# Optimization experiments

Hardware: AMD Instinct MI355X
Metric: run time of the kernel (lower is better)

The kernel has to match this reference:

```python
import jax, jax.numpy as jnp
import numpy as np

POOL = 7  # RoIPooling output size (7,7)


def roi_pool(x, img, rois):
    """RoIPool matching the torch loop: scale rois to feature coords, truncate to int,
    take inclusive slice [y1:y2+1, x1:x2+1] and AdaptiveMaxPool2d((7,7)).
    x: [1,C,H,W], img: [1,3,h,w], rois: [N,4] (x1,y1,x2,y2 in image coords).
    Returns [N,C,7,7]."""
    _, C, H, W = x.shape
    h_img, w_img = img.shape[2], img.shape[3]
    scale = jnp.array([W / w_img, H / h_img, W / w_img, H / h_img], jnp.float32)
    r = (rois * scale).astype(jnp.int32)  # .long() truncation (coords >= 0)
    x1 = jnp.clip(r[:, 0], 0, W - 1)
    y1 = jnp.clip(r[:, 1], 0, H - 1)
    x2 = jnp.clip(r[:, 2], 0, W - 1)
    y2 = jnp.clip(r[:, 3], 0, H - 1)
    ww = x2 - x1 + 1  # inclusive slice width
    hh = y2 - y1 + 1
    i = jnp.arange(POOL)
    # AdaptiveMaxPool bin boundaries: start=floor(i*L/7), end=ceil((i+1)*L/7)  -> [N,7]
    col_s = x1[:, None] + (i[None, :] * ww[:, None]) // POOL
    col_e = x1[:, None] + ((i[None, :] + 1) * ww[:, None] + POOL - 1) // POOL
    row_s = y1[:, None] + (i[None, :] * hh[:, None]) // POOL
    row_e = y1[:, None] + ((i[None, :] + 1) * hh[:, None] + POOL - 1) // POOL
    wpos = jnp.arange(W)
    hpos = jnp.arange(H)
    colmask = (wpos[None, None, :] >= col_s[:, :, None]) & (wpos[None, None, :] < col_e[:, :, None])  # [N,7,W]
    rowmask = (hpos[None, None, :] >= row_s[:, :, None]) & (hpos[None, None, :] < row_e[:, :, None])  # [N,7,H]
    feat = x[0]  # [C,H,W]
    neg = jnp.asarray(jnp.finfo(feat.dtype).min, feat.dtype)
    def per_roi(masks):
        rm, cm = masks  # [7,H], [7,W]
        # separable max over the rectangular bin: cols first, then rows
        t = jnp.max(jnp.where(cm[None, None, :, :], feat[:, :, None, :], neg), axis=-1)  # [C,H,7]
        return jnp.max(jnp.where(rm[None, :, :, None], t[:, None, :, :], neg), axis=2)  # [C,7,7]
    return jax.lax.map(per_roi, (rowmask, colmask))  # [N,C,7,7]


def setup_inputs() -> dict:
    key = jax.random.key(0)
    ks = jax.random.split(key, 10)
    C, H, W = 512, 50, 50
    h_img, w_img = 800, 800
    N = 512
    num_classes = 20
    x = jax.random.normal(ks[0], (1, C, H, W), jnp.float32)
    img = jnp.zeros((1, 3, h_img, w_img), jnp.float32)
    bx = jax.random.uniform(ks[1], (N,), minval=0.0, maxval=w_img - 320.0)
    by = jax.random.uniform(ks[2], (N,), minval=0.0, maxval=h_img - 320.0)
    bw = jax.random.uniform(ks[3], (N,), minval=32.0, maxval=320.0)
    bh = jax.random.uniform(ks[4], (N,), minval=32.0, maxval=320.0)
    rois = jnp.stack([bx, by, bx + bw, by + bh], axis=1).astype(jnp.float32)
    D = C * POOL * POOL  # 25088
    W1 = jax.random.normal(ks[5], (D, 4096), jnp.float32) / np.sqrt(D)
    b1 = jnp.zeros((4096,), jnp.float32)
    W2 = jax.random.normal(ks[6], (4096, 4096), jnp.float32) / np.sqrt(4096)
    b2 = jnp.zeros((4096,), jnp.float32)
    Wcls = jax.random.normal(ks[7], (4096, num_classes + 1), jnp.float32) / np.sqrt(4096)
    bcls = jnp.zeros((num_classes + 1,), jnp.float32)
    Wreg = jax.random.normal(ks[8], (4096, 4 * (num_classes + 1)), jnp.float32) / np.sqrt(4096)
    breg = jnp.zeros((4 * (num_classes + 1),), jnp.float32)
    return {"x": x, "img": img, "rois": rois, "W1": W1, "b1": b1, "W2": W2,
            "b2": b2, "Wcls": Wcls, "bcls": bcls, "Wreg": Wreg, "breg": breg}


def reference(x, img, rois, W1, b1, W2, b2, Wcls, bcls, Wreg, breg):
    pooled = roi_pool(x, img, rois)                 # [N,C,7,7]
    f = pooled.reshape(pooled.shape[0], -1)          # flatten -> [N,25088]
    f = jax.nn.relu(f @ W1 + b1)                     # fc_head layer 1
    f = jax.nn.relu(f @ W2 + b2)                     # fc_head layer 2
    y_cls = f @ Wcls + bcls                          # [N, num_classes+1]
    y_reg = f @ Wreg + breg                          # [N, 4*(num_classes+1)]
    return (y_cls, y_reg)
```

## Files before the change

kernel.cpp:

```cpp
#include <hip/hip_runtime.h>


typedef __attribute__((ext_vector_type(8))) __bf16 bf16x8;
typedef __attribute__((ext_vector_type(4))) float f32x4;

#define N_ROIS 512
#define FH 50
#define FW 50
#define KK1 25088
#define D1 4096
#define BK 32

__device__ __forceinline__ void gll16(const void* g, void* l) {
  __builtin_amdgcn_global_load_lds(
      (const __attribute__((address_space(1))) void*)g,
      (__attribute__((address_space(3))) void*)l, 16, 0, 0);
}

__global__ __launch_bounds__(256) void roipool_kernel(
    const float* __restrict__ x, const float* __restrict__ rois,
    __bf16* __restrict__ pooled) {
  const int bid = blockIdx.x;
  const int roi = bid >> 3;
  const int cg = bid & 7;
  const float s = 0.0625f;
  const float r0 = rois[roi * 4 + 0], r1 = rois[roi * 4 + 1];
  const float r2 = rois[roi * 4 + 2], r3 = rois[roi * 4 + 3];
  int x1 = (int)(r0 * s); x1 = min(max(x1, 0), FW - 1);
  int y1 = (int)(r1 * s); y1 = min(max(y1, 0), FH - 1);
  int x2 = (int)(r2 * s); x2 = min(max(x2, 0), FW - 1);
  int y2 = (int)(r3 * s); y2 = min(max(y2, 0), FH - 1);
  const int ww = x2 - x1 + 1, hh = y2 - y1 + 1;
  __shared__ int cs[7], ce[7], rs[7], re[7];
  if (threadIdx.x < 7) {
    int i = threadIdx.x;
    cs[i] = x1 + (i * ww) / 7;
    ce[i] = x1 + ((i + 1) * ww + 6) / 7;
    rs[i] = y1 + (i * hh) / 7;
    re[i] = y1 + ((i + 1) * hh + 6) / 7;
  }
  __syncthreads();
  for (int idx = threadIdx.x; idx < 64 * 49; idx += 256) {
    int cl = idx / 49;
    int p = idx - cl * 49;
    int py = p / 7, px = p - py * 7;
    const int c = cg * 64 + cl;
    const float* base = x + (size_t)c * (FH * FW);
    float m = -3.402823466e38f;
    for (int y = rs[py]; y < re[py]; ++y) {
      const float* rowp = base + y * FW;
      for (int xx = cs[px]; xx < ce[px]; ++xx) m = fmaxf(m, rowp[xx]);
    }
    pooled[(size_t)roi * KK1 + c * 49 + p] = (__bf16)m;
  }
}

template <typename OutT>
__global__ __launch_bounds__(256, 1) void gemm_pipe(
    const __bf16* __restrict__ A, const float* __restrict__ B,
    OutT* __restrict__ part, int N, int K, int kslice, int npad, int zshift) {
  __shared__ float Blds[4][32 * 128];
  const int tid = threadIdx.x;
  const int lane = tid & 63;
  const int w = tid >> 6;
  const int bid = blockIdx.x;
  const int z = bid & ((1 << zshift) - 1);
  const int n0 = (bid >> zshift) * 128;
  const int kbeg = z * kslice;
  const int niters = kslice / BK;
  const int fr = lane & 15;
  const int ks = lane >> 4;

  f32x4 acc[8][8];
#pragma unroll
  for (int i = 0; i < 8; ++i)
#pragma unroll
    for (int j = 0; j < 8; ++j) acc[i][j] = (f32x4){0.f, 0.f, 0.f, 0.f};

  const __bf16* Abase = A + (size_t)(w * 128 + fr) * K + kbeg + ks * 8;
  const size_t Astride = (size_t)16 * K;

  const int srow = w * 8 + (lane >> 5);
  const float* Bsrc = B + n0 + (((lane & 31) ^ (2 * w)) << 2);

  bf16x8 af[8];

#define STAGE(t)                                                          \
  {                                                                       \
    int off = (t) * BK;                                                   \
    if (off >= kslice) off = 0;    \
    _Pragma("unroll") for (int i = 0; i < 4; ++i) {                       \
      gll16((const void*)(Bsrc + (size_t)(kbeg + off + srow + 2 * i) * N),\
            (void*)&Blds[(t) & 3][(w * 8 + 2 * i) * 128]);                \
    }                                                                     \
  }

#define RD8(P, nf_)                                                       \
  {                                                                       \
    const int base_ = (ks * 8) * 128 +                                    \
        ((((nf_) * 4 + (fr >> 2)) ^ (2 * ks)) << 2) + (fr & 3);           \
    P##0 = bl[base_];        P##1 = bl[base_ + 128];                      \
    P##2 = bl[base_ + 256];  P##3 = bl[base_ + 384];                      \
    P##4 = bl[base_ + 512];  P##5 = bl[base_ + 640];                      \
    P##6 = bl[base_ + 768];  P##7 = bl[base_ + 896];                      \
  }

#define MM8(P, nf_)                                                       \
  {                                                                       \
    bf16x8 bfr;                                                           \
    bfr[0] = (__bf16)P##0; bfr[1] = (__bf16)P##1;                         \
    bfr[2] = (__bf16)P##2; bfr[3] = (__bf16)P##3;                         \
    bfr[4] = (__bf16)P##4; bfr[5] = (__bf16)P##5;                         \
    bfr[6] = (__bf16)P##6; bfr[7] = (__bf16)P##7;                         \
    _Pragma("unroll") for (int mf = 0; mf < 8; ++mf)                      \
        acc[mf][nf_] = __builtin_amdgcn_mfma_f32_16x16x32_bf16(           \
            af[mf], bfr, acc[mf][nf_], 0, 0, 0);                          \
  }

  STAGE(0);
  STAGE(1);

  for (int it = 0; it < niters; ++it) {
    {
      const __bf16* ap = Abase + (size_t)it * BK;
#pragma unroll
      for (int i = 0; i < 8; ++i)
        af[i] = *(const bf16x8*)(ap + (size_t)i * Astride);
    }
    STAGE(it + 2);
    asm volatile("s_waitcnt vmcnt(16)" ::: "memory");
    __builtin_amdgcn_s_barrier();
    __builtin_amdgcn_sched_barrier(0);

    const float* bl = &Blds[it & 3][0];
    float rA0, rA1, rA2, rA3, rA4, rA5, rA6, rA7;
    float rB0, rB1, rB2, rB3, rB4, rB5, rB6, rB7;
    float rC0, rC1, rC2, rC3, rC4, rC5, rC6, rC7;
    RD8(rA, 0);
    RD8(rB, 1);
    RD8(rC, 2); MM8(rA, 0);
    RD8(rA, 3); MM8(rB, 1);
    RD8(rB, 4); MM8(rC, 2);
    RD8(rC, 5); MM8(rA, 3);
    RD8(rA, 6); MM8(rB, 4);
    RD8(rB, 7); MM8(rC, 5);
    MM8(rA, 6);
    MM8(rB, 7);
  }
#undef MM8
#undef RD8
#undef STAGE

  const int r0 = ks * 4;
  OutT* pbase = part + (size_t)z * 512 * npad;
#pragma unroll
  for (int mf = 0; mf < 8; ++mf)
#pragma unroll
    for (int nf = 0; nf < 8; ++nf) {
      const int col = n0 + nf * 16 + fr;
#pragma unroll
      for (int r = 0; r < 4; ++r) {
        const int row = w * 128 + mf * 16 + r0 + r;
        pbase[(size_t)row * npad + col] = (OutT)acc[mf][nf][r];
      }
    }
}

template <typename OutT>
__global__ __launch_bounds__(256, 1) void gemm_small(
    const __bf16* __restrict__ A, const float* __restrict__ B,
    OutT* __restrict__ part, int N, int K, int kslice, int npad, int zshift) {
  const int tid = threadIdx.x;
  const int lane = tid & 63;
  const int w = tid >> 6;
  const int bid = blockIdx.x;
  const int z = bid & ((1 << zshift) - 1);
  const int n0 = (bid >> zshift) * 64;
  const int kbeg = z * kslice;
  const int niters = kslice / BK;
  const int kmax = kbeg + kslice;
  const int fr = lane & 15;
  const int ks = lane >> 4;
  const int m0 = w * 128;
  const bool fullN = (n0 + 64) <= N;

  f32x4 acc[8][4];
#pragma unroll
  for (int i = 0; i < 8; ++i)
#pragma unroll
    for (int j = 0; j < 4; ++j) acc[i][j] = (f32x4){0.f, 0.f, 0.f, 0.f};

  const __bf16* Abase = A + (size_t)(m0 + fr) * K + ks * 8;
  const size_t Astride = (size_t)16 * K;
  const float* Bbase = B + n0 + fr;

  bf16x8 afA[8], afB[8];
  float bA[32], bB[32];

#define LOAD_A(D, t)                                                     \
  {                                                                      \
    int kk = kbeg + (t) * BK;                                            \
    if (kk >= kmax) kk = kbeg;                                           \
    const __bf16* ap = Abase + kk;                                       \
    _Pragma("unroll") for (int i = 0; i < 8; ++i)                        \
        D[i] = *(const bf16x8*)(ap + (size_t)i * Astride);               \
  }

#define LOAD_B(S, t)                                                     \
  {                                                                      \
    int kg = kbeg + (t) * BK;                                            \
    if (kg >= kmax) kg = kbeg;                                           \
    const float* p = Bbase + (size_t)(kg + ks * 8) * N;                  \
    if (fullN) {                                                         \
      _Pragma("unroll") for (int e = 0; e < 8; ++e) {                    \
        _Pragma("unroll") for (int nf = 0; nf < 4; ++nf)                 \
            S[e * 4 + nf] = p[nf * 16];                                  \
        p += N;                                                          \
      }                                                                  \
    } else {                                                             \
      _Pragma("unroll") for (int e = 0; e < 8; ++e) {                    \
        _Pragma("unroll") for (int nf = 0; nf < 4; ++nf)                 \
            S[e * 4 + nf] =                                              \
                (n0 + nf * 16 + fr < N) ? p[nf * 16] : 0.f;              \
        p += N;                                                          \
      }                                                                  \
    }                                                                    \
  }

#define BODY(it, CA, NA, CB)                                             \
  {                                                                      \
    bf16x8 bfr[4];                                                       \
    _Pragma("unroll") for (int e = 0; e < 8; ++e)                        \
        _Pragma("unroll") for (int nf = 0; nf < 4; ++nf)                 \
            bfr[nf][e] = (__bf16)CB[e * 4 + nf];                         \
    LOAD_B(CB, (it) + 2);                                                \
    LOAD_A(NA, (it) + 1);                                                \
    _Pragma("unroll") for (int nf = 0; nf < 4; ++nf)                     \
        _Pragma("unroll") for (int mf = 0; mf < 8; ++mf)                 \
            acc[mf][nf] = __builtin_amdgcn_mfma_f32_16x16x32_bf16(       \
                CA[mf], bfr[nf], acc[mf][nf], 0, 0, 0);                  \
  }

  LOAD_A(afA, 0);
  LOAD_B(bA, 0);
  LOAD_B(bB, 1);
  for (int it = 0; it < niters; it += 2) {
    BODY(it, afA, afB, bA);
    BODY(it + 1, afB, afA, bB);
  }
#undef BODY
#undef LOAD_B
#undef LOAD_A

  const int r0 = ks * 4;
  OutT* pbase = part + (size_t)z * 512 * npad;
#pragma unroll
  for (int mf = 0; mf < 8; ++mf)
#pragma unroll
    for (int nf = 0; nf < 4; ++nf) {
      const int col = n0 + nf * 16 + fr;
#pragma unroll
      for (int r = 0; r < 4; ++r) {
        const int row = m0 + mf * 16 + r0 + r;
        pbase[(size_t)row * npad + col] = (OutT)acc[mf][nf][r];
      }
    }
}

__global__ __launch_bounds__(256) void reduce_relu_kernel(
    const __bf16* __restrict__ part, const float* __restrict__ bias,
    __bf16* __restrict__ out, int nsplit) {
  const int idx = blockIdx.x * 256 + threadIdx.x;
  const int flat = idx * 8;
  if (flat >= 512 * 4096) return;
  float s[8];
#pragma unroll
  for (int j = 0; j < 8; ++j) s[j] = 0.f;
  for (int sp = 0; sp < nsplit; ++sp) {
    bf16x8 v = *(const bf16x8*)(part + (size_t)sp * (512 * 4096) + flat);
#pragma unroll
    for (int j = 0; j < 8; ++j) s[j] += (float)v[j];
  }
  const int nb = flat & 4095;
  bf16x8 o;
#pragma unroll
  for (int j = 0; j < 8; ++j) {
    float v = s[j] + bias[nb + j];
    o[j] = (__bf16)(v > 0.f ? v : 0.f);
  }
  *(bf16x8*)(out + flat) = o;
}

__global__ __launch_bounds__(256) void reduce_out_kernel(
    const float* __restrict__ pc, const float* __restrict__ pr,
    const float* __restrict__ bcls, const float* __restrict__ breg,
    float* __restrict__ out, int nsplit) {
  const int gid = blockIdx.x * 256 + threadIdx.x;
  if (gid >= 512 * 105) return;
  if (gid < 512 * 21) {
    const int m = gid / 21, j = gid - m * 21;
    float s = bcls[j];
    for (int sp = 0; sp < nsplit; ++sp)
      s += pc[(size_t)sp * 512 * 128 + m * 128 + j];
    out[gid] = s;
  } else {
    const int g = gid - 512 * 21;
    const int m = g / 84, j = g - m * 84;
    float s = breg[j];
    for (int sp = 0; sp < nsplit; ++sp)
      s += pr[(size_t)sp * 512 * 128 + m * 128 + j];
    out[gid] = s;
  }
}

extern "C" void kernel_launch(void* const* d_in, const int* in_sizes, int n_in,
                              void* d_out, int out_size, void* d_ws, size_t ws_size,
                              hipStream_t stream) {
  (void)in_sizes; (void)n_in; (void)out_size;
  const float* x    = (const float*)d_in[0];
  const float* rois = (const float*)d_in[2];
  const float* W1   = (const float*)d_in[3];
  const float* b1   = (const float*)d_in[4];
  const float* W2   = (const float*)d_in[5];
  const float* b2   = (const float*)d_in[6];
  const float* Wcls = (const float*)d_in[7];
  const float* bcls = (const float*)d_in[8];
  const float* Wreg = (const float*)d_in[9];
  const float* breg = (const float*)d_in[10];
  float* out = (float*)d_out;

  const size_t pooled_b = (size_t)512 * KK1 * 2;
  const size_t act_b = (size_t)512 * D1 * 2;
  const size_t need8 = pooled_b + (size_t)8 * act_b + 2 * act_b;
  const int ns = (ws_size >= need8) ? 8 : 2;
  const int zshift = (ns == 8) ? 3 : 1;

  char* ws = (char*)d_ws;
  __bf16* pooled = (__bf16*)ws;
  __bf16* part1 = (__bf16*)(ws + pooled_b);
  __bf16* f1 = (__bf16*)(ws + pooled_b + (size_t)ns * act_b);
  __bf16* f2 = (__bf16*)(ws + pooled_b + (size_t)ns * act_b + act_b);
  __bf16* part2 = (__bf16*)ws;
  float* pcls = (float*)ws;
  float* preg = (float*)(ws + (size_t)64 * 512 * 128 * 4);

  roipool_kernel<<<N_ROIS * 8, 256, 0, stream>>>(x, rois, pooled);

  gemm_pipe<__bf16><<<32 * ns, 256, 0, stream>>>(
      pooled, W1, part1, 4096, KK1, KK1 / ns, 4096, zshift);
  reduce_relu_kernel<<<1024, 256, 0, stream>>>(part1, b1, f1, ns);

  gemm_pipe<__bf16><<<32 * ns, 256, 0, stream>>>(
      f1, W2, part2, 4096, 4096, 4096 / ns, 4096, zshift);
  reduce_relu_kernel<<<1024, 256, 0, stream>>>(part2, b2, f2, ns);

  gemm_small<float><<<64, 256, 0, stream>>>(
      f2, Wcls, pcls, 21, 4096, 64, 128, 6);
  gemm_small<float><<<128, 256, 0, stream>>>(
      f2, Wreg, preg, 84, 4096, 64, 128, 6);
  reduce_out_kernel<<<(512 * 105 + 255) / 256, 256, 0, stream>>>(
      pcls, preg, bcls, breg, out, 64);
}
```

Baseline: 340.6 us.

## Stage A tiles through double-buffered LDS with async global-to-LDS loads

The A operand (bf16 pooled features) is now brought into a swizzled, double-buffered LDS tile using `global_load_lds`, one stage ahead. Previously it was loaded straight from global memory into registers at the top of every iteration. This is meant to hide A-load latency behind the MFMA work and free registers. The existing `vmcnt` wait now also covers the A stage. The cost is 64KB more LDS per block and extra ds_read traffic for the A fragments.

```diff
diff --git a/kernel.cpp b/kernel.cpp
--- a/kernel.cpp
+++ b/kernel.cpp
@@ -60,6 +60,7 @@
     const __bf16* __restrict__ A, const float* __restrict__ B,
     OutT* __restrict__ part, int N, int K, int kslice, int npad, int zshift) {
   __shared__ float Blds[4][32 * 128];
+  __shared__ __bf16 A_lds[2][512 * 32];
   const int tid = threadIdx.x;
   const int lane = tid & 63;
   const int w = tid >> 6;
@@ -77,15 +78,27 @@
 #pragma unroll
     for (int j = 0; j < 8; ++j) acc[i][j] = (f32x4){0.f, 0.f, 0.f, 0.f};
 
-  const __bf16* Abase = A + (size_t)(w * 128 + fr) * K + kbeg + ks * 8;
-  const size_t Astride = (size_t)16 * K;
+  const int aswz = (lane & 3) ^ ((lane >> 2) & 3) ^ ((lane >> 4) & 3);
+  const __bf16* Asrc =
+      A + (size_t)(w * 128 + (lane >> 2)) * K + kbeg + aswz * 8;
+  const int aslot = ks ^ ((fr & 3) ^ ((fr >> 2) & 3));
 
   const int srow = w * 8 + (lane >> 5);
   const float* Bsrc = B + n0 + (((lane & 31) ^ (2 * w)) << 2);
 
   bf16x8 af[8];
 
-#define STAGE(t)                                                          \
+#define STAGE_A(t)                                                        \
+  {                                                                       \
+    int off = (t) * BK;                                                   \
+    if (off >= kslice) off = 0;    \
+    _Pragma("unroll") for (int i = 0; i < 8; ++i) {                       \
+      gll16((const void*)(Asrc + (size_t)(i * 16) * K + off),             \
+            (void*)&A_lds[(t) & 1][(w * 128 + i * 16) * 32]);             \
+    }                                                                     \
+  }
+
+#define STAGE_B(t)                                                        \
   {                                                                       \
     int off = (t) * BK;                                                   \
     if (off >= kslice) off = 0;    \
@@ -117,21 +130,24 @@
             af[mf], bfr, acc[mf][nf_], 0, 0, 0);                          \
   }
 
-  STAGE(0);
-  STAGE(1);
+  STAGE_A(0);
+  STAGE_B(0);
+  STAGE_B(1);
 
   for (int it = 0; it < niters; ++it) {
-    {
-      const __bf16* ap = Abase + (size_t)it * BK;
-#pragma unroll
-      for (int i = 0; i < 8; ++i)
-        af[i] = *(const bf16x8*)(ap + (size_t)i * Astride);
-    }
-    STAGE(it + 2);
+    STAGE_A(it + 1);
+    STAGE_B(it + 2);
     asm volatile("s_waitcnt vmcnt(16)" ::: "memory");
     __builtin_amdgcn_s_barrier();
     __builtin_amdgcn_sched_barrier(0);
 
+    {
+      const __bf16* al = &A_lds[it & 1][0];
+#pragma unroll
+      for (int mf = 0; mf < 8; ++mf)
+        af[mf] = *(const bf16x8*)(al + (w * 128 + mf * 16 + fr) * 32 +
+                                  aslot * 8);
+    }
     const float* bl = &Blds[it & 3][0];
     float rA0, rA1, rA2, rA3, rA4, rA5, rA6, rA7;
     float rB0, rB1, rB2, rB3, rB4, rB5, rB6, rB7;
@@ -149,7 +165,8 @@
   }
 #undef MM8
 #undef RD8
-#undef STAGE
+#undef STAGE_B
+#undef STAGE_A
 
   const int r0 = ks * 4;
   OutT* pbase = part + (size_t)z * 512 * npad;
```

New measurement: 340.3 us, median of 2. Within noise of the previous version (-0.1%).
